# Kernel tuning notes

Hardware: AMD Instinct MI355X
Metric: run time of the kernel (lower is better)

The kernel has to match this reference:

```python
import jax, jax.numpy as jnp
import numpy as np
from jax import lax

N_NODES = 200000
FEAT = 64
B = 4096
DEG = 32
P = 2048
EMBED = 64
CONTRA = 64
EPS = 1e-8


def _cos(a, b):
    # cosine similarity along last axis, torch-style eps clamp
    num = jnp.sum(a * b, axis=-1)
    na = jnp.sqrt(jnp.sum(a * a, axis=-1))
    nb = jnp.sqrt(jnp.sum(b * b, axis=-1))
    return num / (jnp.maximum(na, EPS) * jnp.maximum(nb, EPS))


def setup_inputs() -> dict:
    key = jax.random.key(0)
    ks = jax.random.split(key, 16)
    return {
        "nodes": jax.random.randint(ks[0], (B,), 0, N_NODES),
        "labels": jax.random.randint(ks[1], (B,), 0, 2),
        "neigh1": jax.random.randint(ks[2], (B, DEG), 0, N_NODES),
        "neigh2": jax.random.randint(ks[3], (B, DEG), 0, N_NODES),
        "neigh3": jax.random.randint(ks[4], (B, DEG), 0, N_NODES),
        "pos_nodes": jax.random.randint(ks[5], (P,), 0, N_NODES),
        "features": jax.random.normal(ks[6], (N_NODES, FEAT), jnp.float32),
        "weight": jax.random.normal(ks[7], (EMBED * 3 + FEAT, EMBED), jnp.float32) * 0.05,
        "rsimTrans": jax.random.normal(ks[8], (FEAT, CONTRA), jnp.float32) * 0.05,
        "pos_embs": jax.random.normal(ks[9], (3, CONTRA), jnp.float32),
        "W1": jax.random.normal(ks[10], (FEAT, EMBED), jnp.float32) * 0.05,
        "W2": jax.random.normal(ks[11], (FEAT, EMBED), jnp.float32) * 0.05,
        "W3": jax.random.normal(ks[12], (FEAT, EMBED), jnp.float32) * 0.05,
        "sample_num": 16,
    }


def _relation(features, rsimTrans, center_orig, center_sim, pos_sim, neigh, pos_emb, W, sample_num):
    n_orig = features[neigh]                               # [B, D, F] irregular gather
    n_sim = jax.nn.relu(jnp.einsum('bdf,fc->bdc', n_orig, rsimTrans))  # [B, D, C]
    neigh_scores = _cos(center_orig[:, None, :], n_orig)   # [B, D]
    neigh_pos_scores = _cos(pos_emb[None, None, :], n_sim) # [B, D]
    pos_scores = _cos(pos_emb[None, :], pos_sim)           # [P]
    center_scores = _cos(pos_emb[None, :], center_sim)     # [B]
    # per-relation sampling: keep top ceil(D*rho) neighbors by pos-similarity
    _, idx = lax.top_k(neigh_pos_scores, sample_num)       # [B, k]
    sampled = jnp.take_along_axis(n_orig, idx[..., None], axis=1)  # [B, k, F]
    agg = jnp.mean(sampled, axis=1)                        # [B, F]
    r_feats = jax.nn.relu(agg @ W)                         # [B, E]
    sampled_pos = jnp.take_along_axis(neigh_pos_scores, idx, axis=1)
    loss = jnp.mean((sampled_pos - jnp.mean(pos_scores)) ** 2)
    return r_feats, loss


def reference(nodes, labels, neigh1, neigh2, neigh3, pos_nodes, features,
              weight, rsimTrans, pos_embs, W1, W2, W3, sample_num):
    center_orig = features[nodes]                              # [B, F]
    center_sim = jax.nn.relu(center_orig @ rsimTrans)          # [B, C]
    pos_sim = jax.nn.relu(features[pos_nodes] @ rsimTrans)     # [P, C]

    r1, l1 = _relation(features, rsimTrans, center_orig, center_sim, pos_sim,
                       neigh1, pos_embs[0], W1, sample_num)
    r2, l2 = _relation(features, rsimTrans, center_orig, center_sim, pos_sim,
                       neigh2, pos_embs[1], W2, sample_num)
    r3, l3 = _relation(features, rsimTrans, center_orig, center_sim, pos_sim,
                       neigh3, pos_embs[2], W3, sample_num)

    cat_feats = jnp.concatenate([center_orig, r1, r2, r3], axis=1)  # [B, F+3E]
    combined = jax.nn.relu(cat_feats @ weight).T                    # [E, B]
    feat_contra_loss = (l1 + l2 + l3) / 3.0
    return combined, feat_contra_loss
```

## Files before the change

### kernel.cpp

```cpp
#include <hip/hip_runtime.h>
#include <hip/hip_bf16.h>

#define NN     200000
#define FEATD  64
#define BN     4096
#define DEG    32
#define PP     2048
#define EMB    64
#define EPSV   1e-8f
#define NTILE64 3125
#define AWAVES  2048

#define WS_SC    0
#define WS_MISC  800000
#define WS_LOSS  800064
#define WS_RF    800832

typedef short  bf16x8 __attribute__((ext_vector_type(8)));
typedef float  f32x4  __attribute__((ext_vector_type(4)));

__device__ __forceinline__ unsigned int bfr(float x) {
    unsigned int u = __float_as_uint(x);
    return (u + 0x7FFFu + ((u >> 16) & 1u)) & 0xFFFF0000u;
}

__global__ __launch_bounds__(256, 2) void node_precompute(
    const float* __restrict__ features, const float* __restrict__ rsim,
    const float* __restrict__ pos_embs, float4* __restrict__ node_sc)
{
    __shared__ unsigned int lds[4][2][8][64][4];
    __shared__ float4 trp[4][16][16];
    int t = threadIdx.x, w = t >> 6, l = t & 63;
    int lg = l >> 4;
    int lr = l & 15;
    const float4* Gf = (const float4*)features;

    bf16x8 rhi[2][4], rlo[2][4];
#pragma unroll
    for (int kk = 0; kk < 2; ++kk)
#pragma unroll
        for (int nf = 0; nf < 4; ++nf) {
            union { unsigned int u[4]; bf16x8 v; } H, L;
#pragma unroll
            for (int i = 0; i < 4; ++i) {
                int k0 = kk * 32 + lg * 8 + i * 2;
                int j  = nf * 16 + lr;
                float x0 = rsim[k0 * 64 + j];
                float x1 = rsim[(k0 + 1) * 64 + j];
                unsigned int r0 = bfr(x0), r1 = bfr(x1);
                H.u[i] = (r0 >> 16) | r1;
                float l0 = x0 - __uint_as_float(r0);
                float l1 = x1 - __uint_as_float(r1);
                L.u[i] = (__float_as_uint(l0) >> 16)
                       | (__float_as_uint(l1) & 0xFFFF0000u);
            }
            rhi[kk][nf] = H.v; rlo[kk][nf] = L.v;
        }

    float pe[3][4];
#pragma unroll
    for (int rr = 0; rr < 3; ++rr)
#pragma unroll
        for (int nf = 0; nf < 4; ++nf)
            pe[rr][nf] = pos_embs[rr * 64 + nf * 16 + lr];

    unsigned int (*Lhi)[64][4] = lds[w][0];
    unsigned int (*Llo)[64][4] = lds[w][1];
    float4 (*T)[16] = trp[w];

    float4 vv[16];
    int tile = blockIdx.x * 4 + w;
    if (tile < NTILE64) {
        const float4* src = Gf + (size_t)tile * 1024;
#pragma unroll
        for (int s = 0; s < 16; ++s) vv[s] = src[s * 64 + l];
    }

    for (; tile < NTILE64; tile += AWAVES) {
#pragma unroll
        for (int s = 0; s < 16; ++s) {
            float4 v = vv[s];
            int node = s * 4 + lg;
            int kg = lr >> 1, half = lr & 1;
            unsigned int rx = bfr(v.x), ry = bfr(v.y);
            unsigned int rz = bfr(v.z), rw = bfr(v.w);
            unsigned int h0 = (rx >> 16) | ry;
            unsigned int h1 = (rz >> 16) | rw;
            float lx = v.x - __uint_as_float(rx), ly = v.y - __uint_as_float(ry);
            float lz = v.z - __uint_as_float(rz), lw = v.w - __uint_as_float(rw);
            unsigned int l0 = (__float_as_uint(lx) >> 16)
                            | (__float_as_uint(ly) & 0xFFFF0000u);
            unsigned int l1 = (__float_as_uint(lz) >> 16)
                            | (__float_as_uint(lw) & 0xFFFF0000u);
            uint2* dh = (uint2*)&Lhi[kg][node ^ kg][half * 2];
            uint2* dl = (uint2*)&Llo[kg][node ^ kg][half * 2];
            *dh = make_uint2(h0, h1);
            *dl = make_uint2(l0, l1);
        }

        int nt = tile + AWAVES;
        if (nt < NTILE64) {
            const float4* src = Gf + (size_t)nt * 1024;
#pragma unroll
            for (int s = 0; s < 16; ++s) vv[s] = src[s * 64 + l];
        }

        const bf16x8* ph = (const bf16x8*)Lhi;
        const bf16x8* pl = (const bf16x8*)Llo;

#pragma unroll
        for (int mf = 0; mf < 4; ++mf) {
            int node = mf * 16 + lr;
            bf16x8 ah0 = ph[lg * 64 + (node ^ lg)];
            bf16x8 ah1 = ph[(4 + lg) * 64 + (node ^ (4 + lg))];
            bf16x8 al0 = pl[lg * 64 + (node ^ lg)];
            bf16x8 al1 = pl[(4 + lg) * 64 + (node ^ (4 + lg))];

            f32x4 acc[4];
#pragma unroll
            for (int nf = 0; nf < 4; ++nf) acc[nf] = (f32x4)(0.f);
#pragma unroll
            for (int nf = 0; nf < 4; ++nf) {
                acc[nf] = __builtin_amdgcn_mfma_f32_16x16x32_bf16(
                              ah0, rhi[0][nf], acc[nf], 0, 0, 0);
                acc[nf] = __builtin_amdgcn_mfma_f32_16x16x32_bf16(
                              ah1, rhi[1][nf], acc[nf], 0, 0, 0);
                acc[nf] = __builtin_amdgcn_mfma_f32_16x16x32_bf16(
                              ah0, rlo[0][nf], acc[nf], 0, 0, 0);
                acc[nf] = __builtin_amdgcn_mfma_f32_16x16x32_bf16(
                              ah1, rlo[1][nf], acc[nf], 0, 0, 0);
                acc[nf] = __builtin_amdgcn_mfma_f32_16x16x32_bf16(
                              al0, rhi[0][nf], acc[nf], 0, 0, 0);
                acc[nf] = __builtin_amdgcn_mfma_f32_16x16x32_bf16(
                              al1, rhi[1][nf], acc[nf], 0, 0, 0);
            }

#pragma unroll
            for (int reg = 0; reg < 4; ++reg) {
                float s0 = 0.f, s1 = 0.f, s2 = 0.f, q = 0.f;
#pragma unroll
                for (int nf = 0; nf < 4; ++nf) {
                    float v = fmaxf(acc[nf][reg], 0.f);
                    s0 += v * pe[0][nf];
                    s1 += v * pe[1][nf];
                    s2 += v * pe[2][nf];
                    q  += v * v;
                }
                int nd = lg * 4 + reg;
                T[nd][(lr + nd) & 15] = make_float4(s0, s1, s2, q);
            }
            int rn = l >> 2, rq = l & 3;
            float4 a0 = T[rn][(rq * 4 + 0 + rn) & 15];
            float4 a1 = T[rn][(rq * 4 + 1 + rn) & 15];
            float4 a2 = T[rn][(rq * 4 + 2 + rn) & 15];
            float4 a3 = T[rn][(rq * 4 + 3 + rn) & 15];
            float sx = a0.x + a1.x + a2.x + a3.x;
            float sy = a0.y + a1.y + a2.y + a3.y;
            float sz = a0.z + a1.z + a2.z + a3.z;
            float sw = a0.w + a1.w + a2.w + a3.w;
#pragma unroll
            for (int o = 1; o < 4; o <<= 1) {
                sx += __shfl_xor(sx, o);
                sy += __shfl_xor(sy, o);
                sz += __shfl_xor(sz, o);
                sw += __shfl_xor(sw, o);
            }
            if (rq == 0)
                node_sc[tile * 64 + mf * 16 + rn] =
                    make_float4(sx, sy, sz, sqrtf(sw));
        }
    }
}

__global__ __launch_bounds__(1024) void pos_stats(
    const int* __restrict__ pos_nodes, const float4* __restrict__ node_sc,
    const float* __restrict__ pos_embs, float* __restrict__ misc,
    float* __restrict__ lossacc)
{
    __shared__ float invpe_s[3];
    __shared__ float wsum[16][3];
    int t = threadIdx.x, wv = t >> 6, lane = t & 63;

    if (t < 24) lossacc[t * 32] = 0.f;

    float pv = (t < 192) ? pos_embs[t] : 0.f;
    float q = pv * pv;
#pragma unroll
    for (int off = 32; off; off >>= 1) q += __shfl_down(q, off);
    if (t < 192 && lane == 0) {
        float inv = 1.f / fmaxf(sqrtf(q), EPSV);
        invpe_s[wv] = inv;
        misc[4 + wv] = inv;
    }
    __syncthreads();

    float i0 = invpe_s[0], i1 = invpe_s[1], i2 = invpe_s[2];
    float s0 = 0.f, s1 = 0.f, s2 = 0.f;
    for (int p = t; p < PP; p += 1024) {
        int n = pos_nodes[p];
        float4 sc = node_sc[n];
        float invn = 1.f / fmaxf(sc.w, EPSV);
        s0 += sc.x * i0 * invn;
        s1 += sc.y * i1 * invn;
        s2 += sc.z * i2 * invn;
    }
#pragma unroll
    for (int off = 32; off; off >>= 1) {
        s0 += __shfl_down(s0, off);
        s1 += __shfl_down(s1, off);
        s2 += __shfl_down(s2, off);
    }
    if (lane == 0) { wsum[wv][0] = s0; wsum[wv][1] = s1; wsum[wv][2] = s2; }
    __syncthreads();
    if (t < 3) {
        float s = 0.f;
        for (int w = 0; w < 16; ++w) s += wsum[w][t];
        misc[t] = s / (float)PP;
    }
}

__global__ __launch_bounds__(256) void relation_agg(
    const int* __restrict__ n1, const int* __restrict__ n2, const int* __restrict__ n3,
    const float* __restrict__ features, const float4* __restrict__ node_sc,
    const float* __restrict__ W1, const float* __restrict__ W2, const float* __restrict__ W3,
    const float* __restrict__ misc, float* __restrict__ lossacc,
    float* __restrict__ rfeat, const int* __restrict__ smp)
{
    int r = blockIdx.y;
    const int*   neigh = (r == 0) ? n1 : (r == 1) ? n2 : n3;
    const float* W     = (r == 0) ? W1 : (r == 1) ? W2 : W3;
    int k = smp[0];
    int t = threadIdx.x;
    int wv = t >> 6, lane = t & 63;
    int b = blockIdx.x * 4 + wv;
    float inv_pe   = misc[4 + r];
    float mean_pos = misc[r];

    __shared__ int sel_ids[4][32];
    __shared__ float4 aggl[4][16];

    float s = -1e30f;
    int   n = 0;
    if (lane < 32) {
        n = neigh[b * DEG + lane];
        float4 sc = node_sc[n];
        float num = (r == 0) ? sc.x : (r == 1) ? sc.y : sc.z;
        s = num * inv_pe / fmaxf(sc.w, EPSV);
    }
    int cnt = 0;
#pragma unroll
    for (int d2 = 0; d2 < 32; ++d2) {
        float v = __shfl(s, d2);
        cnt += ((v > s) || (v == s && d2 < lane)) ? 1 : 0;
    }
    bool sel = (lane < 32) && (cnt < k);
    if (sel) sel_ids[wv][cnt] = n;

    float lv = sel ? (s - mean_pos) * (s - mean_pos) : 0.f;
#pragma unroll
    for (int off = 32; off; off >>= 1) lv += __shfl_down(lv, off);
    if (lane == 0)
        atomicAdd(&lossacc[(r * 8 + (blockIdx.x & 7)) * 32], lv);

    const float4* F = (const float4*)features;
    int col   = lane & 15;
    int rbase = lane >> 4;
    float4 a = make_float4(0.f, 0.f, 0.f, 0.f);
    if (k == 16) {
        int nid0 = sel_ids[wv][rbase];
        int nid1 = sel_ids[wv][rbase + 4];
        int nid2 = sel_ids[wv][rbase + 8];
        int nid3 = sel_ids[wv][rbase + 12];
        float4 v0 = F[(size_t)nid0 * 16 + col];
        float4 v1 = F[(size_t)nid1 * 16 + col];
        float4 v2 = F[(size_t)nid2 * 16 + col];
        float4 v3 = F[(size_t)nid3 * 16 + col];
        a.x = v0.x + v1.x + v2.x + v3.x;
        a.y = v0.y + v1.y + v2.y + v3.y;
        a.z = v0.z + v1.z + v2.z + v3.z;
        a.w = v0.w + v1.w + v2.w + v3.w;
    } else {
        for (int row0 = 0; row0 < k; row0 += 4) {
            int row = row0 + rbase;
            if (row < k) {
                int nid = sel_ids[wv][row];
                float4 v = F[(size_t)nid * 16 + col];
                a.x += v.x; a.y += v.y; a.z += v.z; a.w += v.w;
            }
        }
    }
#pragma unroll
    for (int off = 16; off <= 32; off <<= 1) {
        a.x += __shfl_xor(a.x, off);
        a.y += __shfl_xor(a.y, off);
        a.z += __shfl_xor(a.z, off);
        a.w += __shfl_xor(a.w, off);
    }
    float inv_k = 1.f / (float)k;
    a.x *= inv_k; a.y *= inv_k; a.z *= inv_k; a.w *= inv_k;

    if (lane < 16) aggl[wv][lane] = a;

    float acc = 0.f;
#pragma unroll
    for (int j4 = 0; j4 < 16; ++j4) {
        float4 ag = aggl[wv][j4];
        acc += ag.x * W[(j4 * 4 + 0) * EMB + lane]
             + ag.y * W[(j4 * 4 + 1) * EMB + lane]
             + ag.z * W[(j4 * 4 + 2) * EMB + lane]
             + ag.w * W[(j4 * 4 + 3) * EMB + lane];
    }
    rfeat[((size_t)r * BN + b) * EMB + lane] = fmaxf(acc, 0.f);
}

#define CSTRIDE 264
__global__ __launch_bounds__(256) void final_mm(
    const int* __restrict__ nodes, const float* __restrict__ features,
    const float* __restrict__ rfeat, const float* __restrict__ weight,
    const float* __restrict__ lossacc, const int* __restrict__ smp,
    float* __restrict__ out)
{
    __shared__ float cat_b[8 * CSTRIDE];
    __shared__ float trans[8 * 65];
    __shared__ float ls[24];
    int t = threadIdx.x;
    int b0 = blockIdx.x * 8;

    if (blockIdx.x == 0 && t < 24) ls[t] = lossacc[t * 32];

    for (int idx = t; idx < 512; idx += 256) {
        int bb = idx >> 6, f = idx & 63;
        cat_b[bb * CSTRIDE + f] = features[(size_t)nodes[b0 + bb] * FEATD + f];
    }
#pragma unroll
    for (int r = 0; r < 3; ++r)
        for (int idx = t; idx < 512; idx += 256) {
            int bb = idx >> 6, j = idx & 63;
            cat_b[bb * CSTRIDE + 64 + r * 64 + j] =
                rfeat[((size_t)r * BN + b0 + bb) * EMB + j];
        }
    __syncthreads();

    int wv = t >> 6, lane = t & 63;
    int bb0 = wv * 2;
    float acc0 = 0.f, acc1 = 0.f;
    const float* c0p = &cat_b[bb0 * CSTRIDE];
    const float* c1p = &cat_b[(bb0 + 1) * CSTRIDE];
    for (int i0 = 0; i0 < 256; i0 += 16) {
        float w[16];
#pragma unroll
        for (int u = 0; u < 16; ++u)
            w[u] = weight[(i0 + u) * EMB + lane];
#pragma unroll
        for (int u = 0; u < 16; ++u) {
            acc0 += w[u] * c0p[i0 + u];
            acc1 += w[u] * c1p[i0 + u];
        }
    }
    trans[bb0 * 65 + lane]       = fmaxf(acc0, 0.f);
    trans[(bb0 + 1) * 65 + lane] = fmaxf(acc1, 0.f);
    __syncthreads();

    for (int idx = t; idx < 512; idx += 256) {
        int e = idx >> 3, bb = idx & 7;
        out[(size_t)e * BN + b0 + bb] = trans[bb * 65 + e];
    }

    if (blockIdx.x == 0 && t == 0) {
        int k = smp[0];
        float s = 0.f;
        for (int i = 0; i < 24; ++i) s += ls[i];
        out[(size_t)EMB * BN] = s / (3.f * (float)BN * (float)k);
    }
}

extern "C" void kernel_launch(void* const* d_in, const int* in_sizes, int n_in,
                              void* d_out, int out_size, void* d_ws, size_t ws_size,
                              hipStream_t stream) {
    const int*   nodes     = (const int*)  d_in[0];
    const int*   neigh1    = (const int*)  d_in[2];
    const int*   neigh2    = (const int*)  d_in[3];
    const int*   neigh3    = (const int*)  d_in[4];
    const int*   pos_nodes = (const int*)  d_in[5];
    const float* features  = (const float*)d_in[6];
    const float* weight    = (const float*)d_in[7];
    const float* rsim      = (const float*)d_in[8];
    const float* pos_embs  = (const float*)d_in[9];
    const float* W1        = (const float*)d_in[10];
    const float* W2        = (const float*)d_in[11];
    const float* W3        = (const float*)d_in[12];
    const int*   smp       = (const int*)  d_in[13];
    float* out = (float*)d_out;
    float* ws  = (float*)d_ws;

    float4* node_sc = (float4*)(ws + WS_SC);
    float*  misc    = ws + WS_MISC;
    float*  lossacc = ws + WS_LOSS;
    float*  rfeat   = ws + WS_RF;

    node_precompute<<<dim3(512), dim3(256), 0, stream>>>(
        features, rsim, pos_embs, node_sc);
    pos_stats<<<dim3(1), dim3(1024), 0, stream>>>(
        pos_nodes, node_sc, pos_embs, misc, lossacc);
    relation_agg<<<dim3(BN / 4, 3), dim3(256), 0, stream>>>(
        neigh1, neigh2, neigh3, features, node_sc, W1, W2, W3,
        misc, lossacc, rfeat, smp);
    final_mm<<<dim3(BN / 8), dim3(256), 0, stream>>>(
        nodes, features, rfeat, weight, lossacc, smp, out);
}
```

Baseline: 68.26 us.

## Remove pos_stats kernel, expand loss algebraically, and fold stats into final kernel

Drops the single-block pos_stats launch. relation_agg now computes the pos-embedding norm itself and writes per-wave sums of s and s² instead of atomically accumulating (s-mean)², so the positive-node mean no longer has to be known before relation_agg runs. Block 0 of final_mm computes the positive-node mean and reduces the partial sums, using the expanded form of the squared difference to get the loss. node_precompute also switches from a persistent, prefetching 2048-wave loop to one tile per wave over more blocks. This saves one serial launch and the atomics, but block 0 of final_mm does extra serial work, and the expanded variance is less numerically stable.

Measured after the change: 70.14 us. 2.8% more time.

```diff
diff --git a/kernel.cpp b/kernel.cpp
--- a/kernel.cpp
+++ b/kernel.cpp
@@ -9,12 +9,10 @@
 #define EMB    64
 #define EPSV   1e-8f
 #define NTILE64 3125
-#define AWAVES  2048
 
 #define WS_SC    0
-#define WS_MISC  800000
-#define WS_LOSS  800064
-#define WS_RF    800832
+#define WS_PL    1000000
+#define WS_RF    1100000
 
 typedef short  bf16x8 __attribute__((ext_vector_type(8)));
 typedef float  f32x4  __attribute__((ext_vector_type(4)));
@@ -31,6 +29,8 @@
     __shared__ unsigned int lds[4][2][8][64][4];
     __shared__ float4 trp[4][16][16];
     int t = threadIdx.x, w = t >> 6, l = t & 63;
+    int tile = blockIdx.x * 4 + w;
+    if (tile >= NTILE64) return;
     int lg = l >> 4;
     int lr = l & 15;
     const float4* Gf = (const float4*)features;
@@ -68,154 +68,91 @@
     unsigned int (*Llo)[64][4] = lds[w][1];
     float4 (*T)[16] = trp[w];
 
-    float4 vv[16];
-    int tile = blockIdx.x * 4 + w;
-    if (tile < NTILE64) {
-        const float4* src = Gf + (size_t)tile * 1024;
-#pragma unroll
-        for (int s = 0; s < 16; ++s) vv[s] = src[s * 64 + l];
-    }
-
-    for (; tile < NTILE64; tile += AWAVES) {
-#pragma unroll
-        for (int s = 0; s < 16; ++s) {
-            float4 v = vv[s];
-            int node = s * 4 + lg;
-            int kg = lr >> 1, half = lr & 1;
-            unsigned int rx = bfr(v.x), ry = bfr(v.y);
-            unsigned int rz = bfr(v.z), rw = bfr(v.w);
-            unsigned int h0 = (rx >> 16) | ry;
-            unsigned int h1 = (rz >> 16) | rw;
-            float lx = v.x - __uint_as_float(rx), ly = v.y - __uint_as_float(ry);
-            float lz = v.z - __uint_as_float(rz), lw = v.w - __uint_as_float(rw);
-            unsigned int l0 = (__float_as_uint(lx) >> 16)
-                            | (__float_as_uint(ly) & 0xFFFF0000u);
-            unsigned int l1 = (__float_as_uint(lz) >> 16)
-                            | (__float_as_uint(lw) & 0xFFFF0000u);
-            uint2* dh = (uint2*)&Lhi[kg][node ^ kg][half * 2];
-            uint2* dl = (uint2*)&Llo[kg][node ^ kg][half * 2];
-            *dh = make_uint2(h0, h1);
-            *dl = make_uint2(l0, l1);
-        }
-
-        int nt = tile + AWAVES;
-        if (nt < NTILE64) {
-            const float4* src = Gf + (size_t)nt * 1024;
-#pragma unroll
-            for (int s = 0; s < 16; ++s) vv[s] = src[s * 64 + l];
-        }
-
-        const bf16x8* ph = (const bf16x8*)Lhi;
-        const bf16x8* pl = (const bf16x8*)Llo;
-
-#pragma unroll
-        for (int mf = 0; mf < 4; ++mf) {
-            int node = mf * 16 + lr;
-            bf16x8 ah0 = ph[lg * 64 + (node ^ lg)];
-            bf16x8 ah1 = ph[(4 + lg) * 64 + (node ^ (4 + lg))];
-            bf16x8 al0 = pl[lg * 64 + (node ^ lg)];
-            bf16x8 al1 = pl[(4 + lg) * 64 + (node ^ (4 + lg))];
-
-            f32x4 acc[4];
-#pragma unroll
-            for (int nf = 0; nf < 4; ++nf) acc[nf] = (f32x4)(0.f);
+    const float4* src = Gf + (size_t)tile * 1024;
+#pragma unroll
+    for (int s = 0; s < 16; ++s) {
+        float4 v = src[s * 64 + l];
+        int node = s * 4 + lg;
+        int kg = lr >> 1, half = lr & 1;
+        unsigned int rx = bfr(v.x), ry = bfr(v.y);
+        unsigned int rz = bfr(v.z), rw = bfr(v.w);
+        unsigned int h0 = (rx >> 16) | ry;
+        unsigned int h1 = (rz >> 16) | rw;
+        float lx = v.x - __uint_as_float(rx), ly = v.y - __uint_as_float(ry);
+        float lz = v.z - __uint_as_float(rz), lw = v.w - __uint_as_float(rw);
+        unsigned int l0 = (__float_as_uint(lx) >> 16)
+                        | (__float_as_uint(ly) & 0xFFFF0000u);
+        unsigned int l1 = (__float_as_uint(lz) >> 16)
+                        | (__float_as_uint(lw) & 0xFFFF0000u);
+        uint2* dh = (uint2*)&Lhi[kg][node ^ kg][half * 2];
+        uint2* dl = (uint2*)&Llo[kg][node ^ kg][half * 2];
+        *dh = make_uint2(h0, h1);
+        *dl = make_uint2(l0, l1);
+    }
+
+    const bf16x8* ph = (const bf16x8*)Lhi;
+    const bf16x8* pl = (const bf16x8*)Llo;
+
+#pragma unroll
+    for (int mf = 0; mf < 4; ++mf) {
+        int node = mf * 16 + lr;
+        bf16x8 ah0 = ph[lg * 64 + (node ^ lg)];
+        bf16x8 ah1 = ph[(4 + lg) * 64 + (node ^ (4 + lg))];
+        bf16x8 al0 = pl[lg * 64 + (node ^ lg)];
+        bf16x8 al1 = pl[(4 + lg) * 64 + (node ^ (4 + lg))];
+
+        f32x4 acc[4];
+#pragma unroll
+        for (int nf = 0; nf < 4; ++nf) acc[nf] = (f32x4)(0.f);
+#pragma unroll
+        for (int nf = 0; nf < 4; ++nf) {
+            acc[nf] = __builtin_amdgcn_mfma_f32_16x16x32_bf16(
+                          ah0, rhi[0][nf], acc[nf], 0, 0, 0);
+            acc[nf] = __builtin_amdgcn_mfma_f32_16x16x32_bf16(
+                          ah1, rhi[1][nf], acc[nf], 0, 0, 0);
+            acc[nf] = __builtin_amdgcn_mfma_f32_16x16x32_bf16(
+                          ah0, rlo[0][nf], acc[nf], 0, 0, 0);
+            acc[nf] = __builtin_amdgcn_mfma_f32_16x16x32_bf16(
+                          ah1, rlo[1][nf], acc[nf], 0, 0, 0);
+            acc[nf] = __builtin_amdgcn_mfma_f32_16x16x32_bf16(
+                          al0, rhi[0][nf], acc[nf], 0, 0, 0);
+            acc[nf] = __builtin_amdgcn_mfma_f32_16x16x32_bf16(
+                          al1, rhi[1][nf], acc[nf], 0, 0, 0);
+        }
+
+#pragma unroll
+        for (int reg = 0; reg < 4; ++reg) {
+            float s0 = 0.f, s1 = 0.f, s2 = 0.f, q = 0.f;
 #pragma unroll
             for (int nf = 0; nf < 4; ++nf) {
-                acc[nf] = __builtin_amdgcn_mfma_f32_16x16x32_bf16(
-                              ah0, rhi[0][nf], acc[nf], 0, 0, 0);
-                acc[nf] = __builtin_amdgcn_mfma_f32_16x16x32_bf16(
-                              ah1, rhi[1][nf], acc[nf], 0, 0, 0);
-                acc[nf] = __builtin_amdgcn_mfma_f32_16x16x32_bf16(
-                              ah0, rlo[0][nf], acc[nf], 0, 0, 0);
-                acc[nf] = __builtin_amdgcn_mfma_f32_16x16x32_bf16(
-                              ah1, rlo[1][nf], acc[nf], 0, 0, 0);
-                acc[nf] = __builtin_amdgcn_mfma_f32_16x16x32_bf16(
-                              al0, rhi[0][nf], acc[nf], 0, 0, 0);
-                acc[nf] = __builtin_amdgcn_mfma_f32_16x16x32_bf16(
-                              al1, rhi[1][nf], acc[nf], 0, 0, 0);
+                float v = fmaxf(acc[nf][reg], 0.f);
+                s0 += v * pe[0][nf];
+                s1 += v * pe[1][nf];
+                s2 += v * pe[2][nf];
+                q  += v * v;
             }
-
-#pragma unroll
-            for (int reg = 0; reg < 4; ++reg) {
-                float s0 = 0.f, s1 = 0.f, s2 = 0.f, q = 0.f;
-#pragma unroll
-                for (int nf = 0; nf < 4; ++nf) {
-                    float v = fmaxf(acc[nf][reg], 0.f);
-                    s0 += v * pe[0][nf];
-                    s1 += v * pe[1][nf];
-                    s2 += v * pe[2][nf];
-                    q  += v * v;
-                }
-                int nd = lg * 4 + reg;
-                T[nd][(lr + nd) & 15] = make_float4(s0, s1, s2, q);
-            }
-            int rn = l >> 2, rq = l & 3;
-            float4 a0 = T[rn][(rq * 4 + 0 + rn) & 15];
-            float4 a1 = T[rn][(rq * 4 + 1 + rn) & 15];
-            float4 a2 = T[rn][(rq * 4 + 2 + rn) & 15];
-            float4 a3 = T[rn][(rq * 4 + 3 + rn) & 15];
-            float sx = a0.x + a1.x + a2.x + a3.x;
-            float sy = a0.y + a1.y + a2.y + a3.y;
-            float sz = a0.z + a1.z + a2.z + a3.z;
-            float sw = a0.w + a1.w + a2.w + a3.w;
-#pragma unroll
-            for (int o = 1; o < 4; o <<= 1) {
-                sx += __shfl_xor(sx, o);
-                sy += __shfl_xor(sy, o);
-                sz += __shfl_xor(sz, o);
-                sw += __shfl_xor(sw, o);
-            }
-            if (rq == 0)
-                node_sc[tile * 64 + mf * 16 + rn] =
-                    make_float4(sx, sy, sz, sqrtf(sw));
-        }
-    }
-}
-
-__global__ __launch_bounds__(1024) void pos_stats(
-    const int* __restrict__ pos_nodes, const float4* __restrict__ node_sc,
-    const float* __restrict__ pos_embs, float* __restrict__ misc,
-    float* __restrict__ lossacc)
-{
-    __shared__ float invpe_s[3];
-    __shared__ float wsum[16][3];
-    int t = threadIdx.x, wv = t >> 6, lane = t & 63;
-
-    if (t < 24) lossacc[t * 32] = 0.f;
-
-    float pv = (t < 192) ? pos_embs[t] : 0.f;
-    float q = pv * pv;
-#pragma unroll
-    for (int off = 32; off; off >>= 1) q += __shfl_down(q, off);
-    if (t < 192 && lane == 0) {
-        float inv = 1.f / fmaxf(sqrtf(q), EPSV);
-        invpe_s[wv] = inv;
-        misc[4 + wv] = inv;
-    }
-    __syncthreads();
-
-    float i0 = invpe_s[0], i1 = invpe_s[1], i2 = invpe_s[2];
-    float s0 = 0.f, s1 = 0.f, s2 = 0.f;
-    for (int p = t; p < PP; p += 1024) {
-        int n = pos_nodes[p];
-        float4 sc = node_sc[n];
-        float invn = 1.f / fmaxf(sc.w, EPSV);
-        s0 += sc.x * i0 * invn;
-        s1 += sc.y * i1 * invn;
-        s2 += sc.z * i2 * invn;
-    }
-#pragma unroll
-    for (int off = 32; off; off >>= 1) {
-        s0 += __shfl_down(s0, off);
-        s1 += __shfl_down(s1, off);
-        s2 += __shfl_down(s2, off);
-    }
-    if (lane == 0) { wsum[wv][0] = s0; wsum[wv][1] = s1; wsum[wv][2] = s2; }
-    __syncthreads();
-    if (t < 3) {
-        float s = 0.f;
-        for (int w = 0; w < 16; ++w) s += wsum[w][t];
-        misc[t] = s / (float)PP;
+            int nd = lg * 4 + reg;
+            T[nd][(lr + nd) & 15] = make_float4(s0, s1, s2, q);
+        }
+        int rn = l >> 2, rq = l & 3;
+        float4 a0 = T[rn][(rq * 4 + 0 + rn) & 15];
+        float4 a1 = T[rn][(rq * 4 + 1 + rn) & 15];
+        float4 a2 = T[rn][(rq * 4 + 2 + rn) & 15];
+        float4 a3 = T[rn][(rq * 4 + 3 + rn) & 15];
+        float sx = a0.x + a1.x + a2.x + a3.x;
+        float sy = a0.y + a1.y + a2.y + a3.y;
+        float sz = a0.z + a1.z + a2.z + a3.z;
+        float sw = a0.w + a1.w + a2.w + a3.w;
+#pragma unroll
+        for (int o = 1; o < 4; o <<= 1) {
+            sx += __shfl_xor(sx, o);
+            sy += __shfl_xor(sy, o);
+            sz += __shfl_xor(sz, o);
+            sw += __shfl_xor(sw, o);
+        }
+        if (rq == 0)
+            node_sc[tile * 64 + mf * 16 + rn] =
+                make_float4(sx, sy, sz, sqrtf(sw));
     }
 }
 
@@ -223,7 +160,7 @@
     const int* __restrict__ n1, const int* __restrict__ n2, const int* __restrict__ n3,
     const float* __restrict__ features, const float4* __restrict__ node_sc,
     const float* __restrict__ W1, const float* __restrict__ W2, const float* __restrict__ W3,
-    const float* __restrict__ misc, float* __restrict__ lossacc,
+    const float* __restrict__ pos_embs, float* __restrict__ plossws,
     float* __restrict__ rfeat, const int* __restrict__ smp)
 {
     int r = blockIdx.y;
@@ -233,11 +170,15 @@
     int t = threadIdx.x;
     int wv = t >> 6, lane = t & 63;
     int b = blockIdx.x * 4 + wv;
-    float inv_pe   = misc[4 + r];
-    float mean_pos = misc[r];
 
     __shared__ int sel_ids[4][32];
     __shared__ float4 aggl[4][16];
+
+    float pv = pos_embs[r * 64 + lane];
+    float qq = pv * pv;
+#pragma unroll
+    for (int o = 1; o < 64; o <<= 1) qq += __shfl_xor(qq, o);
+    float inv_pe = 1.f / fmaxf(sqrtf(qq), EPSV);
 
     float s = -1e30f;
     int   n = 0;
@@ -256,11 +197,18 @@
     bool sel = (lane < 32) && (cnt < k);
     if (sel) sel_ids[wv][cnt] = n;
 
-    float lv = sel ? (s - mean_pos) * (s - mean_pos) : 0.f;
-#pragma unroll
-    for (int off = 32; off; off >>= 1) lv += __shfl_down(lv, off);
-    if (lane == 0)
-        atomicAdd(&lossacc[(r * 8 + (blockIdx.x & 7)) * 32], lv);
+    float sp = sel ? s : 0.f;
+    float sq = sel ? s * s : 0.f;
+#pragma unroll
+    for (int off = 32; off; off >>= 1) {
+        sp += __shfl_down(sp, off);
+        sq += __shfl_down(sq, off);
+    }
+    if (lane == 0) {
+        int wid = (r * 1024 + blockIdx.x) * 4 + wv;
+        plossws[wid * 2]     = sp;
+        plossws[wid * 2 + 1] = sq;
+    }
 
     const float4* F = (const float4*)features;
     int col   = lane & 15;
@@ -317,16 +265,18 @@
 __global__ __launch_bounds__(256) void final_mm(
     const int* __restrict__ nodes, const float* __restrict__ features,
     const float* __restrict__ rfeat, const float* __restrict__ weight,
-    const float* __restrict__ lossacc, const int* __restrict__ smp,
-    float* __restrict__ out)
+    const float* __restrict__ pos_embs, const int* __restrict__ pos_nodes,
+    const float4* __restrict__ node_sc, const float* __restrict__ plossws,
+    const int* __restrict__ smp, float* __restrict__ out)
 {
     __shared__ float cat_b[8 * CSTRIDE];
     __shared__ float trans[8 * 65];
-    __shared__ float ls[24];
+    __shared__ float invpe_sm[3];
+    __shared__ float wsum[4][3];
+    __shared__ float lsum[4][3][2];
     int t = threadIdx.x;
+    int wv = t >> 6, lane = t & 63;
     int b0 = blockIdx.x * 8;
-
-    if (blockIdx.x == 0 && t < 24) ls[t] = lossacc[t * 32];
 
     for (int idx = t; idx < 512; idx += 256) {
         int bb = idx >> 6, f = idx & 63;
@@ -341,7 +291,6 @@
         }
     __syncthreads();
 
-    int wv = t >> 6, lane = t & 63;
     int bb0 = wv * 2;
     float acc0 = 0.f, acc1 = 0.f;
     const float* c0p = &cat_b[bb0 * CSTRIDE];
@@ -366,11 +315,61 @@
         out[(size_t)e * BN + b0 + bb] = trans[bb * 65 + e];
     }
 
-    if (blockIdx.x == 0 && t == 0) {
+    if (blockIdx.x != 0) return;
+
+    float pv = (t < 192) ? pos_embs[t] : 0.f;
+    float q = pv * pv;
+#pragma unroll
+    for (int o = 1; o < 64; o <<= 1) q += __shfl_xor(q, o);
+    if (t < 192 && lane == 0)
+        invpe_sm[wv] = 1.f / fmaxf(sqrtf(q), EPSV);
+    __syncthreads();
+
+    float m0 = 0.f, m1 = 0.f, m2 = 0.f;
+    for (int p = t; p < PP; p += 256) {
+        int n = pos_nodes[p];
+        float4 sc = node_sc[n];
+        float invn = 1.f / fmaxf(sc.w, EPSV);
+        m0 += sc.x * invpe_sm[0] * invn;
+        m1 += sc.y * invpe_sm[1] * invn;
+        m2 += sc.z * invpe_sm[2] * invn;
+    }
+#pragma unroll
+    for (int o = 1; o < 64; o <<= 1) {
+        m0 += __shfl_xor(m0, o);
+        m1 += __shfl_xor(m1, o);
+        m2 += __shfl_xor(m2, o);
+    }
+    if (lane == 0) { wsum[wv][0] = m0; wsum[wv][1] = m1; wsum[wv][2] = m2; }
+
+    if (wv < 3) {
+        float s1 = 0.f, s2 = 0.f;
+        const float2* pl2 = (const float2*)plossws;
+        for (int i = lane; i < 4096; i += 64) {
+            float2 v = pl2[wv * 4096 + i];
+            s1 += v.x; s2 += v.y;
+        }
+#pragma unroll
+        for (int o = 1; o < 64; o <<= 1) {
+            s1 += __shfl_xor(s1, o);
+            s2 += __shfl_xor(s2, o);
+        }
+        if (lane == 0) { lsum[0][wv][0] = s1; lsum[0][wv][1] = s2; }
+    }
+    __syncthreads();
+
+    if (t == 0) {
         int k = smp[0];
-        float s = 0.f;
-        for (int i = 0; i < 24; ++i) s += ls[i];
-        out[(size_t)EMB * BN] = s / (3.f * (float)BN * (float)k);
+        float N = (float)BN * (float)k;
+        float loss = 0.f;
+#pragma unroll
+        for (int r = 0; r < 3; ++r) {
+            float mp = (wsum[0][r] + wsum[1][r] + wsum[2][r] + wsum[3][r])
+                       / (float)PP;
+            float s1 = lsum[0][r][0], s2 = lsum[0][r][1];
+            loss += s2 / N - 2.f * mp * s1 / N + mp * mp;
+        }
+        out[(size_t)EMB * BN] = loss / 3.f;
     }
 }
 
@@ -394,17 +393,15 @@
     float* ws  = (float*)d_ws;
 
     float4* node_sc = (float4*)(ws + WS_SC);
-    float*  misc    = ws + WS_MISC;
-    float*  lossacc = ws + WS_LOSS;
+    float*  plossws = ws + WS_PL;
     float*  rfeat   = ws + WS_RF;
 
-    node_precompute<<<dim3(512), dim3(256), 0, stream>>>(
+    node_precompute<<<dim3((NTILE64 + 3) / 4), dim3(256), 0, stream>>>(
         features, rsim, pos_embs, node_sc);
-    pos_stats<<<dim3(1), dim3(1024), 0, stream>>>(
-        pos_nodes, node_sc, pos_embs, misc, lossacc);
     relation_agg<<<dim3(BN / 4, 3), dim3(256), 0, stream>>>(
         neigh1, neigh2, neigh3, features, node_sc, W1, W2, W3,
-        misc, lossacc, rfeat, smp);
+        pos_embs, plossws, rfeat, smp);
     final_mm<<<dim3(BN / 8), dim3(256), 0, stream>>>(
-        nodes, features, rfeat, weight, lossacc, smp, out);
+        nodes, features, rfeat, weight, pos_embs, pos_nodes,
+        node_sc, plossws, smp, out);
 }
```
